# Optimization experiments

Measured on AMD Instinct MI355X. Metric: run time of the kernel, lower is better.

## Reference

```python
import jax, jax.numpy as jnp
import numpy as np

B, T, E, H, V, ENC, ATT = 128, 25, 512, 1024, 32000, 400, 256


def setup_inputs() -> dict:
    key = jax.random.key(0)
    ks = jax.random.split(key, 16)
    s = 0.02
    return {
        "features": jax.random.normal(ks[0], (B, ENC), jnp.float32),
        "captions": jax.random.randint(ks[1], (B, T), 0, V),
        "emb_W": jax.random.normal(ks[2], (V, E), jnp.float32) * s,
        "W_ih": jax.random.normal(ks[3], (4 * H, E + ENC), jnp.float32) * s,
        "W_hh": jax.random.normal(ks[4], (4 * H, H), jnp.float32) * s,
        "b_ih": jnp.zeros((4 * H,), jnp.float32),
        "b_hh": jnp.zeros((4 * H,), jnp.float32),
        "enc_W": jax.random.normal(ks[5], (ATT, ENC), jnp.float32) * s,
        "enc_b": jnp.zeros((ATT,), jnp.float32),
        "dec_W": jax.random.normal(ks[6], (ATT, H), jnp.float32) * s,
        "dec_b": jnp.zeros((ATT,), jnp.float32),
        "full_W": jax.random.normal(ks[7], (1, ATT), jnp.float32) * s,
        "full_b": jnp.zeros((1,), jnp.float32),
        "fcn_W": jax.random.normal(ks[8], (V, H), jnp.float32) * s,
        "fcn_b": jnp.zeros((V,), jnp.float32),
    }


def reference(features, captions, emb_W, W_ih, W_hh, b_ih, b_hh,
              enc_W, enc_b, dec_W, dec_b, full_W, full_b, fcn_W, fcn_b):
    Bsz, hs = features.shape[0], W_hh.shape[1]
    # word embeddings: t=0 uses token id 1 (<SOS>), then teacher-forced captions[:, :-1]
    start = jnp.broadcast_to(emb_W[1][None, None, :], (Bsz, 1, emb_W.shape[1]))
    words = jnp.concatenate([start, emb_W[captions[:, :-1]]], axis=1)  # [B, T, E]
    # encoder_out has a single pixel -> precompute its attention projection once
    att1 = features @ enc_W.T + enc_b  # [B, ATT]
    h0 = jnp.zeros((Bsz, hs), features.dtype)  # tanh(0) == 0
    c0 = jnp.zeros((Bsz, hs), features.dtype)

    def step(carry, w_t):  # w_t: [B, E]
        h, c = carry
        att2 = h @ dec_W.T + dec_b  # [B, ATT]
        score = jax.nn.relu(att1 + att2) @ full_W[0] + full_b[0]  # [B]
        alpha = jax.nn.softmax(score[:, None], axis=1)  # [B, 1] (single pixel -> all ones)
        context = features * alpha  # [B, ENC]
        x = jnp.concatenate([w_t, context], axis=1)
        gates = x @ W_ih.T + b_ih + h @ W_hh.T + b_hh  # [B, 4H]
        i, f, g, o = jnp.split(gates, 4, axis=1)  # torch LSTMCell gate order
        c_new = jax.nn.sigmoid(f) * c + jax.nn.sigmoid(i) * jnp.tanh(g)
        h_new = jax.nn.sigmoid(o) * jnp.tanh(c_new)
        out = h_new @ fcn_W.T + fcn_b  # dropout is identity in eval mode
        return (h_new, c_new), out

    _, outs = jax.lax.scan(step, (h0, c0), jnp.swapaxes(words, 0, 1))  # [T, B, V]
    return jnp.swapaxes(outs, 0, 1)[:, 1:, :]  # [B, T-1, V]
```

## Files before the change

kernel.cpp:

```cpp
#include <hip/hip_runtime.h>
#include <cstdint>

typedef unsigned short ushort_t;
typedef __bf16 bf16x8 __attribute__((ext_vector_type(8)));
typedef float f32x4 __attribute__((ext_vector_type(4)));


__device__ __forceinline__ ushort_t f2bf(float f) {
    unsigned u = __float_as_uint(f);
    unsigned r = (u + 0x7fffu + ((u >> 16) & 1u)) >> 16;
    return (ushort_t)r;
}


__global__ void cvt4(const float* __restrict__ S, ushort_t* __restrict__ D, int n) {
    int i = (blockIdx.x * 256 + threadIdx.x) * 4;
    if (i >= n) return;
    float4 v = *(const float4*)(S + i);
    ushort4 o;
    o.x = f2bf(v.x); o.y = f2bf(v.y); o.z = f2bf(v.z); o.w = f2bf(v.w);
    *(ushort4*)(D + i) = o;
}

__global__ void cvt_wih(const float* __restrict__ W, ushort_t* __restrict__ D) {
    int idx = blockIdx.x * 256 + threadIdx.x;
    int row = idx >> 10, col = idx & 1023;
    D[idx] = (col < 912) ? f2bf(W[row * 912 + col]) : (ushort_t)0;
}

__global__ void build_xall(const float* __restrict__ features, const int* __restrict__ captions,
                           const float* __restrict__ embW, ushort_t* __restrict__ X) {
    int idx = blockIdx.x * 256 + threadIdx.x;
    int r = idx >> 10, col = idx & 1023;
    int t = r >> 7, b = r & 127;
    float v;
    if (col < 512) {
        int tok = (t == 0) ? 1 : captions[b * 25 + (t - 1)];
        v = embW[tok * 512 + col];
    } else if (col < 912) {
        v = features[b * 400 + (col - 512)];
    } else {
        v = 0.f;
    }
    X[idx] = f2bf(v);
}

__global__ void lstm_cell(const float* __restrict__ gates,
                          const float* __restrict__ bi, const float* __restrict__ bh,
                          float* __restrict__ c, ushort_t* __restrict__ h_cur,
                          ushort_t* __restrict__ Hall, int t) {
    int idx = blockIdx.x * 256 + threadIdx.x;
    int b = idx >> 10, u = idx & 1023;
    const float* g = gates + b * 4096;
    float vi = g[u]        + bi[u]        + bh[u];
    float vf = g[u + 1024] + bi[u + 1024] + bh[u + 1024];
    float vg = g[u + 2048] + bi[u + 2048] + bh[u + 2048];
    float vo = g[u + 3072] + bi[u + 3072] + bh[u + 3072];
    float si = 1.f / (1.f + expf(-vi));
    float sf = 1.f / (1.f + expf(-vf));
    float so = 1.f / (1.f + expf(-vo));
    float cn = sf * c[idx] + si * tanhf(vg);
    float hn = so * tanhf(cn);
    c[idx] = cn;
    ushort_t hb = f2bf(hn);
    h_cur[idx] = hb;
    if (t >= 1) Hall[(t - 1) * 131072 + idx] = hb;
}

__global__ __launch_bounds__(256)
void gemm_bt(const ushort_t* __restrict__ A, const ushort_t* __restrict__ B,
             float* __restrict__ C, const float* __restrict__ addsrc,
             const float* __restrict__ bias, int K, int mode) {
    const int ldc  = gridDim.x * 128;
    const int bm   = blockIdx.y, bn = blockIdx.x;
    const int tid  = threadIdx.x;
    const int wave = tid >> 6, lane = tid & 63;

    __shared__ __align__(16) ushort_t As[128 * 64];
    __shared__ __align__(16) ushort_t Bs[128 * 64];

    const ushort_t* Ab = A + (size_t)bm * 128 * K;
    const ushort_t* Bb = B + (size_t)bn * 128 * K;

    f32x4 acc[4][4] = {};

    const int wm = (wave & 1) * 64;
    const int wn = (wave >> 1) * 64;

    for (int k0 = 0; k0 < K; k0 += 64) {
#pragma unroll
        for (int ro = 0; ro < 4; ++ro) {
            int L   = ro * 256 + tid;
            int row = L >> 3;
            int cs  = (L & 7) ^ (row & 7);
            const ushort_t* ga = Ab + row * K + k0 + cs * 8;
            const ushort_t* gb = Bb + row * K + k0 + cs * 8;
            __builtin_amdgcn_global_load_lds(
                (const __attribute__((address_space(1))) void*)ga,
                (__attribute__((address_space(3))) void*)(As + L * 8), 16, 0, 0);
            __builtin_amdgcn_global_load_lds(
                (const __attribute__((address_space(1))) void*)gb,
                (__attribute__((address_space(3))) void*)(Bs + L * 8), 16, 0, 0);
        }
        __syncthreads();

#pragma unroll
        for (int kk = 0; kk < 2; ++kk) {
            bf16x8 af[4], bfr[4];
#pragma unroll
            for (int mt = 0; mt < 4; ++mt) {
                int row = wm + mt * 16 + (lane & 15);
                int cc  = (kk * 4 + (lane >> 4)) ^ (row & 7);
                af[mt]  = *(const bf16x8*)(As + row * 64 + cc * 8);
            }
#pragma unroll
            for (int nt = 0; nt < 4; ++nt) {
                int row = wn + nt * 16 + (lane & 15);
                int cc  = (kk * 4 + (lane >> 4)) ^ (row & 7);
                bfr[nt] = *(const bf16x8*)(Bs + row * 64 + cc * 8);
            }
#pragma unroll
            for (int mt = 0; mt < 4; ++mt)
#pragma unroll
                for (int nt = 0; nt < 4; ++nt)
                    acc[mt][nt] = __builtin_amdgcn_mfma_f32_16x16x32_bf16(
                        af[mt], bfr[nt], acc[mt][nt], 0, 0, 0);
        }
        __syncthreads();
    }

    const int r0 = (lane >> 4) * 4;
    const int cn = lane & 15;
#pragma unroll
    for (int mt = 0; mt < 4; ++mt) {
#pragma unroll
        for (int nt = 0; nt < 4; ++nt) {
#pragma unroll
            for (int r = 0; r < 4; ++r) {
                int m  = wm + mt * 16 + r0 + r;
                int n  = wn + nt * 16 + cn;
                int gm = bm * 128 + m;
                int gn = bn * 128 + n;
                float v = acc[mt][nt][r];
                if (mode == 0) {
                    C[(size_t)gm * ldc + gn] = v;
                } else if (mode == 1) {
                    C[(size_t)gm * ldc + gn] = v + addsrc[(size_t)gm * ldc + gn];
                } else {
                    C[(size_t)(gm & 127) * (24 * 32000) + (size_t)(gm >> 7) * 32000 + gn]
                        = v + bias[gn];
                }
            }
        }
    }
}


extern "C" void kernel_launch(void* const* d_in, const int* in_sizes, int n_in,
                              void* d_out, int out_size, void* d_ws, size_t ws_size,
                              hipStream_t stream) {
    const float* features = (const float*)d_in[0];
    const int*   captions = (const int*)d_in[1];
    const float* emb_W    = (const float*)d_in[2];
    const float* W_ih     = (const float*)d_in[3];
    const float* W_hh     = (const float*)d_in[4];
    const float* b_ih     = (const float*)d_in[5];
    const float* b_hh     = (const float*)d_in[6];
    const float* fcn_W    = (const float*)d_in[13];
    const float* fcn_b    = (const float*)d_in[14];
    float* out = (float*)d_out;

    char* p = (char*)d_ws;
    auto alloc = [&](size_t bytes) { void* r = p; p += bytes; return r; };
    ushort_t* Xall     = (ushort_t*)alloc((size_t)3200 * 1024 * 2);
    ushort_t* Wihb     = (ushort_t*)alloc((size_t)4096 * 1024 * 2);
    ushort_t* Whhb     = (ushort_t*)alloc((size_t)4096 * 1024 * 2);
    ushort_t* Fcnb     = (ushort_t*)alloc((size_t)32000 * 1024 * 2);
    float*    gates_in = (float*)alloc((size_t)3200 * 4096 * 4);
    float*    gates_bf = (float*)alloc((size_t)128 * 4096 * 4);
    ushort_t* Hall     = (ushort_t*)alloc((size_t)3072 * 1024 * 2);
    ushort_t* h_cur    = (ushort_t*)alloc((size_t)128 * 1024 * 2);
    float*    cbuf     = (float*)alloc((size_t)128 * 1024 * 4);
    (void)ws_size; (void)n_in; (void)in_sizes; (void)out_size;

    hipMemsetAsync(h_cur, 0, (size_t)128 * 1024 * 2, stream);
    hipMemsetAsync(cbuf,  0, (size_t)128 * 1024 * 4, stream);

    build_xall<<<(3200 * 1024) / 256, 256, 0, stream>>>(features, captions, emb_W, Xall);
    cvt_wih<<<(4096 * 1024) / 256, 256, 0, stream>>>(W_ih, Wihb);
    cvt4<<<(4096 * 1024) / 1024, 256, 0, stream>>>(W_hh, Whhb, 4096 * 1024);
    cvt4<<<(32000 * 1024) / 1024, 256, 0, stream>>>(fcn_W, Fcnb, 32000 * 1024);

    gemm_bt<<<dim3(32, 25), 256, 0, stream>>>(Xall, Wihb, gates_in, nullptr, nullptr, 1024, 0);

    for (int t = 0; t < 25; ++t) {
        gemm_bt<<<dim3(32, 1), 256, 0, stream>>>(h_cur, Whhb, gates_bf,
                                                 gates_in + (size_t)t * 128 * 4096,
                                                 nullptr, 1024, 1);
        lstm_cell<<<512, 256, 0, stream>>>(gates_bf, b_ih, b_hh, cbuf, h_cur, Hall, t);
    }

    gemm_bt<<<dim3(250, 24), 256, 0, stream>>>(Hall, Fcnb, out, nullptr, fcn_b, 1024, 2);
}
```

Measured before the change: 1.892 ms.

## Fuse recurrent GEMM with LSTM cell via gate-interleaved weights

Reorders W_ih, W_hh and bias rows so each 128-wide output tile holds i,f,g,o for 32 hidden units, enabling a per-step kernel that computes h@W_hh, adds precomputed input gates, and applies the LSTM cell in shared memory. This removes the separate cell kernel launch and the global round trip for step gates each timestep, and folds biases into the input-projection GEMM. The output GEMM also remaps blocks across XCDs for cache locality. It adds a large shared-memory buffer per block, and the per-step kernel still uses only 32 blocks.

```diff
diff --git a/kernel.cpp b/kernel.cpp
--- a/kernel.cpp
+++ b/kernel.cpp
@@ -24,8 +24,23 @@
 
 __global__ void cvt_wih(const float* __restrict__ W, ushort_t* __restrict__ D) {
     int idx = blockIdx.x * 256 + threadIdx.x;
-    int row = idx >> 10, col = idx & 1023;
-    D[idx] = (col < 912) ? f2bf(W[row * 912 + col]) : (ushort_t)0;
+    int p = idx >> 10, col = idx & 1023;
+    int orig = (p & 3) * 1024 + (p >> 2);
+    D[idx] = (col < 912) ? f2bf(W[orig * 912 + col]) : (ushort_t)0;
+}
+
+__global__ void cvt_whh(const float* __restrict__ W, ushort_t* __restrict__ D) {
+    int idx = blockIdx.x * 256 + threadIdx.x;
+    int p = idx >> 10, col = idx & 1023;
+    int orig = (p & 3) * 1024 + (p >> 2);
+    D[idx] = f2bf(W[orig * 1024 + col]);
+}
+
+__global__ void bias_prep(const float* __restrict__ bi, const float* __restrict__ bh,
+                          float* __restrict__ bc) {
+    int p = blockIdx.x * 256 + threadIdx.x;
+    int orig = (p & 3) * 1024 + (p >> 2);
+    bc[p] = bi[orig] + bh[orig];
 }
 
 __global__ void build_xall(const float* __restrict__ features, const int* __restrict__ captions,
@@ -45,34 +60,19 @@
     X[idx] = f2bf(v);
 }
 
-__global__ void lstm_cell(const float* __restrict__ gates,
-                          const float* __restrict__ bi, const float* __restrict__ bh,
-                          float* __restrict__ c, ushort_t* __restrict__ h_cur,
-                          ushort_t* __restrict__ Hall, int t) {
-    int idx = blockIdx.x * 256 + threadIdx.x;
-    int b = idx >> 10, u = idx & 1023;
-    const float* g = gates + b * 4096;
-    float vi = g[u]        + bi[u]        + bh[u];
-    float vf = g[u + 1024] + bi[u + 1024] + bh[u + 1024];
-    float vg = g[u + 2048] + bi[u + 2048] + bh[u + 2048];
-    float vo = g[u + 3072] + bi[u + 3072] + bh[u + 3072];
-    float si = 1.f / (1.f + expf(-vi));
-    float sf = 1.f / (1.f + expf(-vf));
-    float so = 1.f / (1.f + expf(-vo));
-    float cn = sf * c[idx] + si * tanhf(vg);
-    float hn = so * tanhf(cn);
-    c[idx] = cn;
-    ushort_t hb = f2bf(hn);
-    h_cur[idx] = hb;
-    if (t >= 1) Hall[(t - 1) * 131072 + idx] = hb;
-}
-
 __global__ __launch_bounds__(256)
 void gemm_bt(const ushort_t* __restrict__ A, const ushort_t* __restrict__ B,
              float* __restrict__ C, const float* __restrict__ addsrc,
              const float* __restrict__ bias, int K, int mode) {
     const int ldc  = gridDim.x * 128;
-    const int bm   = blockIdx.y, bn = blockIdx.x;
+    int bm = blockIdx.y, bn = blockIdx.x;
+    if (mode == 2) {
+        int id  = blockIdx.y * gridDim.x + blockIdx.x;
+        int xcd = id & 7;
+        int qq  = id >> 3;
+        bm = xcd * 3 + (qq % 3);
+        bn = qq / 3;
+    }
     const int tid  = threadIdx.x;
     const int wave = tid >> 6, lane = tid & 63;
 
@@ -146,12 +146,107 @@
                     C[(size_t)gm * ldc + gn] = v;
                 } else if (mode == 1) {
                     C[(size_t)gm * ldc + gn] = v + addsrc[(size_t)gm * ldc + gn];
+                } else if (mode == 3) {
+                    C[(size_t)gm * ldc + gn] = v + bias[gn];
                 } else {
                     C[(size_t)(gm & 127) * (24 * 32000) + (size_t)(gm >> 7) * 32000 + gn]
                         = v + bias[gn];
                 }
             }
         }
+    }
+}
+
+__global__ __launch_bounds__(256)
+void lstm_step(const ushort_t* __restrict__ hin, const ushort_t* __restrict__ Whh,
+               const float* __restrict__ gin, float* __restrict__ c,
+               ushort_t* __restrict__ hout) {
+    const int bn   = blockIdx.x;
+    const int tid  = threadIdx.x;
+    const int wave = tid >> 6, lane = tid & 63;
+    const int K = 1024;
+
+    __shared__ __align__(16) ushort_t As[128 * 64];
+    __shared__ __align__(16) ushort_t Bs[128 * 64];
+    __shared__ __align__(16) float    gt[128 * 132];
+
+    const ushort_t* Ab = hin;
+    const ushort_t* Bb = Whh + (size_t)bn * 128 * K;
+
+    f32x4 acc[4][4] = {};
+    const int wm = (wave & 1) * 64;
+    const int wn = (wave >> 1) * 64;
+
+    for (int k0 = 0; k0 < K; k0 += 64) {
+#pragma unroll
+        for (int ro = 0; ro < 4; ++ro) {
+            int L   = ro * 256 + tid;
+            int row = L >> 3;
+            int cs  = (L & 7) ^ (row & 7);
+            const ushort_t* ga = Ab + row * K + k0 + cs * 8;
+            const ushort_t* gb = Bb + row * K + k0 + cs * 8;
+            __builtin_amdgcn_global_load_lds(
+                (const __attribute__((address_space(1))) void*)ga,
+                (__attribute__((address_space(3))) void*)(As + L * 8), 16, 0, 0);
+            __builtin_amdgcn_global_load_lds(
+                (const __attribute__((address_space(1))) void*)gb,
+                (__attribute__((address_space(3))) void*)(Bs + L * 8), 16, 0, 0);
+        }
+        __syncthreads();
+#pragma unroll
+        for (int kk = 0; kk < 2; ++kk) {
+            bf16x8 af[4], bfr[4];
+#pragma unroll
+            for (int mt = 0; mt < 4; ++mt) {
+                int row = wm + mt * 16 + (lane & 15);
+                int cc  = (kk * 4 + (lane >> 4)) ^ (row & 7);
+                af[mt]  = *(const bf16x8*)(As + row * 64 + cc * 8);
+            }
+#pragma unroll
+            for (int nt = 0; nt < 4; ++nt) {
+                int row = wn + nt * 16 + (lane & 15);
+                int cc  = (kk * 4 + (lane >> 4)) ^ (row & 7);
+                bfr[nt] = *(const bf16x8*)(Bs + row * 64 + cc * 8);
+            }
+#pragma unroll
+            for (int mt = 0; mt < 4; ++mt)
+#pragma unroll
+                for (int nt = 0; nt < 4; ++nt)
+                    acc[mt][nt] = __builtin_amdgcn_mfma_f32_16x16x32_bf16(
+                        af[mt], bfr[nt], acc[mt][nt], 0, 0, 0);
+        }
+        __syncthreads();
+    }
+
+    const int r0 = (lane >> 4) * 4;
+    const int cn = lane & 15;
+#pragma unroll
+    for (int mt = 0; mt < 4; ++mt)
+#pragma unroll
+        for (int nt = 0; nt < 4; ++nt)
+#pragma unroll
+            for (int r = 0; r < 4; ++r) {
+                int m = wm + mt * 16 + r0 + r;
+                int n = wn + nt * 16 + cn;
+                gt[m * 132 + n] = acc[mt][nt][r] + gin[(size_t)m * 4096 + bn * 128 + n];
+            }
+    __syncthreads();
+
+    const int q = tid & 31;
+    const int u = bn * 32 + q;
+    const int bbase = (tid >> 5) * 16;
+#pragma unroll
+    for (int i = 0; i < 16; ++i) {
+        int b = bbase + i;
+        float4 g4 = *(const float4*)(gt + b * 132 + q * 4);
+        float si = 1.f / (1.f + expf(-g4.x));
+        float sf = 1.f / (1.f + expf(-g4.y));
+        float so = 1.f / (1.f + expf(-g4.w));
+        int ci = b * 1024 + u;
+        float cnew = sf * c[ci] + si * tanhf(g4.z);
+        float hnew = so * tanhf(cnew);
+        c[ci] = cnew;
+        hout[ci] = f2bf(hnew);
     }
 }
 
@@ -177,27 +272,32 @@
     ushort_t* Whhb     = (ushort_t*)alloc((size_t)4096 * 1024 * 2);
     ushort_t* Fcnb     = (ushort_t*)alloc((size_t)32000 * 1024 * 2);
     float*    gates_in = (float*)alloc((size_t)3200 * 4096 * 4);
-    float*    gates_bf = (float*)alloc((size_t)128 * 4096 * 4);
+    float*    bc       = (float*)alloc((size_t)4096 * 4);
     ushort_t* Hall     = (ushort_t*)alloc((size_t)3072 * 1024 * 2);
-    ushort_t* h_cur    = (ushort_t*)alloc((size_t)128 * 1024 * 2);
+    ushort_t* hzero    = (ushort_t*)alloc((size_t)128 * 1024 * 2);
+    ushort_t* htmp     = (ushort_t*)alloc((size_t)128 * 1024 * 2);
     float*    cbuf     = (float*)alloc((size_t)128 * 1024 * 4);
     (void)ws_size; (void)n_in; (void)in_sizes; (void)out_size;
 
-    hipMemsetAsync(h_cur, 0, (size_t)128 * 1024 * 2, stream);
+    hipMemsetAsync(hzero, 0, (size_t)128 * 1024 * 2, stream);
     hipMemsetAsync(cbuf,  0, (size_t)128 * 1024 * 4, stream);
 
     build_xall<<<(3200 * 1024) / 256, 256, 0, stream>>>(features, captions, emb_W, Xall);
     cvt_wih<<<(4096 * 1024) / 256, 256, 0, stream>>>(W_ih, Wihb);
-    cvt4<<<(4096 * 1024) / 1024, 256, 0, stream>>>(W_hh, Whhb, 4096 * 1024);
+    cvt_whh<<<(4096 * 1024) / 256, 256, 0, stream>>>(W_hh, Whhb);
     cvt4<<<(32000 * 1024) / 1024, 256, 0, stream>>>(fcn_W, Fcnb, 32000 * 1024);
-
-    gemm_bt<<<dim3(32, 25), 256, 0, stream>>>(Xall, Wihb, gates_in, nullptr, nullptr, 1024, 0);
+    bias_prep<<<16, 256, 0, stream>>>(b_ih, b_hh, bc);
+
+    gemm_bt<<<dim3(32, 25), 256, 0, stream>>>(Xall, Wihb, gates_in, nullptr, bc, 1024, 3);
 
     for (int t = 0; t < 25; ++t) {
-        gemm_bt<<<dim3(32, 1), 256, 0, stream>>>(h_cur, Whhb, gates_bf,
-                                                 gates_in + (size_t)t * 128 * 4096,
-                                                 nullptr, 1024, 1);
-        lstm_cell<<<512, 256, 0, stream>>>(gates_bf, b_ih, b_hh, cbuf, h_cur, Hall, t);
+        const ushort_t* hin = (t == 0) ? hzero
+                            : (t == 1) ? htmp
+                            : Hall + (size_t)(t - 2) * 131072;
+        ushort_t* hout = (t == 0) ? htmp : Hall + (size_t)(t - 1) * 131072;
+        lstm_step<<<32, 256, 0, stream>>>(hin, Whhb,
+                                          gates_in + (size_t)t * 128 * 4096,
+                                          cbuf, hout);
     }
 
     gemm_bt<<<dim3(250, 24), 256, 0, stream>>>(Hall, Fcnb, out, nullptr, fcn_b, 1024, 2);
```

New measurement: 1.678 ms. -11.3%, faster.

## Replace per-timestep LSTM launches with persistent kernel and grid barrier

Applied to the files above, without the earlier changes.

The 50 per-step launches (a recurrent GEMM plus a cell kernel each) become one persistent kernel of 256 blocks. Each block keeps its slice of W_hh in registers and computes its gates and the cell update from shared memory. Blocks synchronise between timesteps with an atomic-counter grid barrier. W_ih, W_hh and the biases are permuted so each block's 16 columns hold all four gates for 4 units, and the combined bias is folded into the input-projection GEMM. This removes launch overhead and the per-step reload of W_hh and gate round-trips, but it relies on all 256 blocks being co-resident and adds spin-barrier latency.

```diff
diff --git a/kernel.cpp b/kernel.cpp
--- a/kernel.cpp
+++ b/kernel.cpp
@@ -24,8 +24,23 @@
 
 __global__ void cvt_wih(const float* __restrict__ W, ushort_t* __restrict__ D) {
     int idx = blockIdx.x * 256 + threadIdx.x;
-    int row = idx >> 10, col = idx & 1023;
-    D[idx] = (col < 912) ? f2bf(W[row * 912 + col]) : (ushort_t)0;
+    int p = idx >> 10, col = idx & 1023;
+    int orig = (p & 3) * 1024 + (p >> 2);
+    D[idx] = (col < 912) ? f2bf(W[orig * 912 + col]) : (ushort_t)0;
+}
+
+__global__ void cvt_whh(const float* __restrict__ W, ushort_t* __restrict__ D) {
+    int idx = blockIdx.x * 256 + threadIdx.x;
+    int p = idx >> 10, col = idx & 1023;
+    int orig = (p & 3) * 1024 + (p >> 2);
+    D[idx] = f2bf(W[orig * 1024 + col]);
+}
+
+__global__ void bias_prep(const float* __restrict__ bi, const float* __restrict__ bh,
+                          float* __restrict__ bc) {
+    int p = blockIdx.x * 256 + threadIdx.x;
+    int orig = (p & 3) * 1024 + (p >> 2);
+    bc[p] = bi[orig] + bh[orig];
 }
 
 __global__ void build_xall(const float* __restrict__ features, const int* __restrict__ captions,
@@ -45,34 +60,11 @@
     X[idx] = f2bf(v);
 }
 
-__global__ void lstm_cell(const float* __restrict__ gates,
-                          const float* __restrict__ bi, const float* __restrict__ bh,
-                          float* __restrict__ c, ushort_t* __restrict__ h_cur,
-                          ushort_t* __restrict__ Hall, int t) {
-    int idx = blockIdx.x * 256 + threadIdx.x;
-    int b = idx >> 10, u = idx & 1023;
-    const float* g = gates + b * 4096;
-    float vi = g[u]        + bi[u]        + bh[u];
-    float vf = g[u + 1024] + bi[u + 1024] + bh[u + 1024];
-    float vg = g[u + 2048] + bi[u + 2048] + bh[u + 2048];
-    float vo = g[u + 3072] + bi[u + 3072] + bh[u + 3072];
-    float si = 1.f / (1.f + expf(-vi));
-    float sf = 1.f / (1.f + expf(-vf));
-    float so = 1.f / (1.f + expf(-vo));
-    float cn = sf * c[idx] + si * tanhf(vg);
-    float hn = so * tanhf(cn);
-    c[idx] = cn;
-    ushort_t hb = f2bf(hn);
-    h_cur[idx] = hb;
-    if (t >= 1) Hall[(t - 1) * 131072 + idx] = hb;
-}
-
 __global__ __launch_bounds__(256)
 void gemm_bt(const ushort_t* __restrict__ A, const ushort_t* __restrict__ B,
-             float* __restrict__ C, const float* __restrict__ addsrc,
-             const float* __restrict__ bias, int K, int mode) {
+             float* __restrict__ C, const float* __restrict__ bias, int K, int mode) {
     const int ldc  = gridDim.x * 128;
-    const int bm   = blockIdx.y, bn = blockIdx.x;
+    const int bm = blockIdx.y, bn = blockIdx.x;
     const int tid  = threadIdx.x;
     const int wave = tid >> 6, lane = tid & 63;
 
@@ -142,15 +134,95 @@
                 int gm = bm * 128 + m;
                 int gn = bn * 128 + n;
                 float v = acc[mt][nt][r];
-                if (mode == 0) {
-                    C[(size_t)gm * ldc + gn] = v;
-                } else if (mode == 1) {
-                    C[(size_t)gm * ldc + gn] = v + addsrc[(size_t)gm * ldc + gn];
+                if (mode == 3) {
+                    C[(size_t)gm * ldc + gn] = v + bias[gn];
                 } else {
                     C[(size_t)(gm & 127) * (24 * 32000) + (size_t)(gm >> 7) * 32000 + gn]
                         = v + bias[gn];
                 }
             }
+        }
+    }
+}
+
+#define NBLK 256
+__global__ __launch_bounds__(256, 1)
+void lstm_persistent(const ushort_t* __restrict__ Whh,
+                     const float* __restrict__ gin_all,
+                     ushort_t* __restrict__ hbuf0,
+                     ushort_t* __restrict__ Hall,
+                     int* cnt) {
+    const int bn   = blockIdx.x;
+    const int tid  = threadIdx.x;
+    const int wave = tid >> 6, lane = tid & 63;
+
+    __shared__ __align__(16) float gt[128 * 20];
+    __shared__ float c_s[128 * 4];
+
+    const int colp = bn * 16 + (lane & 15);
+    const int kc   = (lane >> 4) * 8;
+    bf16x8 barr[32];
+#pragma unroll
+    for (int kk = 0; kk < 32; ++kk)
+        barr[kk] = *(const bf16x8*)(Whh + (size_t)colp * 1024 + kk * 32 + kc);
+
+    for (int i = tid; i < 512; i += 256) c_s[i] = 0.f;
+    __syncthreads();
+
+    const int mrow0 = wave * 32;
+    const int r0 = (lane >> 4) * 4;
+    const int cn = lane & 15;
+    const int ul = tid & 3;
+    const int b0 = tid >> 2;
+
+    for (int t = 0; t < 25; ++t) {
+        f32x4 acc0 = {}, acc1 = {};
+        if (t > 0) {
+            const ushort_t* hin = (t == 1) ? hbuf0 : Hall + (size_t)(t - 2) * 131072;
+            const ushort_t* a0 = hin + (size_t)(mrow0 + (lane & 15)) * 1024 + kc;
+            const ushort_t* a1 = a0 + 16 * 1024;
+#pragma unroll
+            for (int kk = 0; kk < 32; ++kk) {
+                bf16x8 af0 = *(const bf16x8*)(a0 + kk * 32);
+                bf16x8 af1 = *(const bf16x8*)(a1 + kk * 32);
+                acc0 = __builtin_amdgcn_mfma_f32_16x16x32_bf16(af0, barr[kk], acc0, 0, 0, 0);
+                acc1 = __builtin_amdgcn_mfma_f32_16x16x32_bf16(af1, barr[kk], acc1, 0, 0, 0);
+            }
+        }
+        const float* gin = gin_all + (size_t)t * 524288;
+#pragma unroll
+        for (int r = 0; r < 4; ++r) {
+            int m0 = mrow0 + r0 + r;
+            int m1 = m0 + 16;
+            gt[m0 * 20 + cn] = acc0[r] + gin[(size_t)m0 * 4096 + bn * 16 + cn];
+            gt[m1 * 20 + cn] = acc1[r] + gin[(size_t)m1 * 4096 + bn * 16 + cn];
+        }
+        __syncthreads();
+
+        ushort_t* hout = (t == 0) ? hbuf0 : Hall + (size_t)(t - 1) * 131072;
+#pragma unroll
+        for (int hh = 0; hh < 2; ++hh) {
+            int b = b0 + hh * 64;
+            float4 g4 = *(const float4*)(gt + b * 20 + ul * 4);
+            float si = 1.f / (1.f + expf(-g4.x));
+            float sf = 1.f / (1.f + expf(-g4.y));
+            float so = 1.f / (1.f + expf(-g4.w));
+            float cnew = sf * c_s[b * 4 + ul] + si * tanhf(g4.z);
+            c_s[b * 4 + ul] = cnew;
+            hout[(size_t)b * 1024 + bn * 4 + ul] = f2bf(so * tanhf(cnew));
+        }
+        __syncthreads();
+
+        if (t < 24) {
+            if (tid == 0) {
+                __threadfence();
+                __hip_atomic_fetch_add(cnt, 1, __ATOMIC_RELEASE, __HIP_MEMORY_SCOPE_AGENT);
+                const int tgt = NBLK * (t + 1);
+                while (__hip_atomic_load(cnt, __ATOMIC_ACQUIRE, __HIP_MEMORY_SCOPE_AGENT) < tgt)
+                    __builtin_amdgcn_s_sleep(2);
+                __threadfence();
+            }
+            __syncthreads();
         }
     }
 }
@@ -177,28 +249,23 @@
     ushort_t* Whhb     = (ushort_t*)alloc((size_t)4096 * 1024 * 2);
     ushort_t* Fcnb     = (ushort_t*)alloc((size_t)32000 * 1024 * 2);
     float*    gates_in = (float*)alloc((size_t)3200 * 4096 * 4);
-    float*    gates_bf = (float*)alloc((size_t)128 * 4096 * 4);
+    float*    bc       = (float*)alloc((size_t)4096 * 4);
     ushort_t* Hall     = (ushort_t*)alloc((size_t)3072 * 1024 * 2);
-    ushort_t* h_cur    = (ushort_t*)alloc((size_t)128 * 1024 * 2);
-    float*    cbuf     = (float*)alloc((size_t)128 * 1024 * 4);
+    ushort_t* hbuf0    = (ushort_t*)alloc((size_t)128 * 1024 * 2);
+    int*      cnt      = (int*)alloc(256);
     (void)ws_size; (void)n_in; (void)in_sizes; (void)out_size;
 
-    hipMemsetAsync(h_cur, 0, (size_t)128 * 1024 * 2, stream);
-    hipMemsetAsync(cbuf,  0, (size_t)128 * 1024 * 4, stream);
+    hipMemsetAsync(cnt, 0, 256, stream);
 
     build_xall<<<(3200 * 1024) / 256, 256, 0, stream>>>(features, captions, emb_W, Xall);
     cvt_wih<<<(4096 * 1024) / 256, 256, 0, stream>>>(W_ih, Wihb);
-    cvt4<<<(4096 * 1024) / 1024, 256, 0, stream>>>(W_hh, Whhb, 4096 * 1024);
+    cvt_whh<<<(4096 * 1024) / 256, 256, 0, stream>>>(W_hh, Whhb);
     cvt4<<<(32000 * 1024) / 1024, 256, 0, stream>>>(fcn_W, Fcnb, 32000 * 1024);
-
-    gemm_bt<<<dim3(32, 25), 256, 0, stream>>>(Xall, Wihb, gates_in, nullptr, nullptr, 1024, 0);
-
-    for (int t = 0; t < 25; ++t) {
-        gemm_bt<<<dim3(32, 1), 256, 0, stream>>>(h_cur, Whhb, gates_bf,
-                                                 gates_in + (size_t)t * 128 * 4096,
-                                                 nullptr, 1024, 1);
-        lstm_cell<<<512, 256, 0, stream>>>(gates_bf, b_ih, b_hh, cbuf, h_cur, Hall, t);
-    }
-
-    gemm_bt<<<dim3(250, 24), 256, 0, stream>>>(Hall, Fcnb, out, nullptr, fcn_b, 1024, 2);
-}
+    bias_prep<<<16, 256, 0, stream>>>(b_ih, b_hh, bc);
+
+    gemm_bt<<<dim3(32, 25), 256, 0, stream>>>(Xall, Wihb, gates_in, bc, 1024, 3);
+
+    lstm_persistent<<<NBLK, 256, 0, stream>>>(Whhb, gates_in, hbuf0, Hall, cnt);
+
+    gemm_bt<<<dim3(250, 24), 256, 0, stream>>>(Hall, Fcnb, out, fcn_b, 1024, 2);
+}
```

Result: faster. 1.691 ms (-10.6%).
